# Optimization experiments

Hardware: AMD Instinct MI355X
Metric: run time of the kernel (lower is better)

The kernel has to match this reference:

```python
import jax, jax.numpy as jnp
import numpy as np

N = 10000      # nodes (= num_spatial_nodes)
E = 320000     # edges
IN = 4         # in_channels
HID = 256      # hidden_channels
H1, C1 = 4, 64 # conv1: heads, per-head out (hidden//heads)
EDIM = 1       # edge_feature_size
EPS = 1e-5


def _layernorm(x, g, b):
    mu = jnp.mean(x, axis=-1, keepdims=True)
    var = jnp.mean(jnp.square(x - mu), axis=-1, keepdims=True)
    return (x - mu) / jnp.sqrt(var + EPS) * g + b


def _gatv2(x, src, dst, ea, Wl, bl, Wr, br, We, att, bias, H, C, n):
    # PyG GATv2Conv: lin_l on source, lin_r on target, lin_edge on edge_attr
    xl = (x @ Wl + bl).reshape(n, H, C)
    xr = (x @ Wr + br).reshape(n, H, C)
    ee = (ea @ We).reshape(-1, H, C)
    m = jax.nn.leaky_relu(xl[src] + xr[dst] + ee, 0.2)   # [E', H, C]
    logit = jnp.einsum('ehc,hc->eh', m, att)             # [E', H]
    # segment softmax over incoming edges of each dst node
    mx = jax.ops.segment_max(logit, dst, num_segments=n)
    ex = jnp.exp(logit - mx[dst])
    den = jax.ops.segment_sum(ex, dst, num_segments=n)
    alpha = ex / den[dst]
    out = jax.ops.segment_sum(xl[src] * alpha[:, :, None], dst, num_segments=n)
    return out.reshape(n, H * C) + bias


def setup_inputs() -> dict:
    key = jax.random.key(0)
    ks = jax.random.split(key, 32)
    gl = lambda k, shape, fan: (jax.random.normal(k, shape, jnp.float32) / np.sqrt(fan)).astype(jnp.float32)
    inp = {}
    inp['x'] = jax.random.normal(ks[0], (N, IN), jnp.float32)
    inp['edge_index'] = jax.random.randint(ks[1], (2, E), 0, N, jnp.int32)
    inp['edge_attr'] = jax.random.normal(ks[2], (E, EDIM), jnp.float32)
    # conv1 (heads=4, out=64, concat -> 256)
    inp['Wl1'] = gl(ks[3], (IN, HID), IN);  inp['bl1'] = jnp.zeros((HID,), jnp.float32)
    inp['Wr1'] = gl(ks[4], (IN, HID), IN);  inp['br1'] = jnp.zeros((HID,), jnp.float32)
    inp['We1'] = gl(ks[5], (EDIM, HID), EDIM)
    inp['att1'] = gl(ks[6], (H1, C1), C1)
    inp['bias1'] = jnp.zeros((HID,), jnp.float32)
    inp['g1'] = jnp.ones((HID,), jnp.float32); inp['be1'] = jnp.zeros((HID,), jnp.float32)
    # conv2 (heads=1, out=256)
    inp['Wl2'] = gl(ks[7], (HID, HID), HID); inp['bl2'] = jnp.zeros((HID,), jnp.float32)
    inp['Wr2'] = gl(ks[8], (HID, HID), HID); inp['br2'] = jnp.zeros((HID,), jnp.float32)
    inp['We2'] = gl(ks[9], (EDIM, HID), EDIM)
    inp['att2'] = gl(ks[10], (1, HID), HID)
    inp['bias2'] = jnp.zeros((HID,), jnp.float32)
    inp['g2'] = jnp.ones((HID,), jnp.float32); inp['be2'] = jnp.zeros((HID,), jnp.float32)
    # policy head
    inp['Wp1'] = gl(ks[11], (HID, HID // 2), HID); inp['bp1'] = jnp.zeros((HID // 2,), jnp.float32)
    inp['Wp2'] = gl(ks[12], (HID // 2, IN), HID // 2); inp['bp2'] = jnp.zeros((IN,), jnp.float32)
    return inp


def reference(x, edge_index, edge_attr,
              Wl1, bl1, Wr1, br1, We1, att1, bias1, g1, be1,
              Wl2, bl2, Wr2, br2, We2, att2, bias2, g2, be2,
              Wp1, bp1, Wp2, bp2):
    src, dst = edge_index[0], edge_index[1]
    # add_self_loops with fill_value='mean': loop edge_attr = mean of incoming edge_attr
    deg = jax.ops.segment_sum(jnp.ones((E,), jnp.float32), dst, num_segments=N)
    loop_attr = jax.ops.segment_sum(edge_attr, dst, num_segments=N) / jnp.maximum(deg, 1.0)[:, None]
    ar = jnp.arange(N, dtype=src.dtype)
    src_a = jnp.concatenate([src, ar]); dst_a = jnp.concatenate([dst, ar])
    ea_a = jnp.concatenate([edge_attr, loop_attr], axis=0)
    h = _gatv2(x, src_a, dst_a, ea_a, Wl1, bl1, Wr1, br1, We1, att1, bias1, H1, C1, N)
    h = jax.nn.relu(_layernorm(h, g1, be1))
    h = _gatv2(h, src_a, dst_a, ea_a, Wl2, bl2, Wr2, br2, We2, att2, bias2, 1, HID, N)
    h = jax.nn.relu(_layernorm(h, g2, be2))
    logits = jax.nn.relu(h @ Wp1 + bp1) @ Wp2 + bp2   # [N, IN]
    return jax.nn.softmax(logits.reshape(1, -1), axis=1)
```

## Files before the change

### kernel.cpp

```cpp
#include <hip/hip_runtime.h>
#include <math.h>

#define N_NODES 10000
#define N_EDGES 320000
#define N_AUG   (N_EDGES + N_NODES)
#define CPK_CAP 330752
#define HID     256

typedef short short8 __attribute__((ext_vector_type(8)));
typedef float floatx16 __attribute__((ext_vector_type(16)));

static __device__ __forceinline__ unsigned bf16rne(float f) {
  unsigned u = __float_as_uint(f);
  return (u + 0x7FFFu + ((u >> 16) & 1u)) >> 16;
}

__global__ void k_deg(const int* __restrict__ dst, const float* __restrict__ ea,
                      int* __restrict__ deg, float* __restrict__ asum) {
  int e = blockIdx.x * blockDim.x + threadIdx.x;
  if (e < N_EDGES) {
    int d = dst[e];
    atomicAdd(&deg[d], 1);
    atomicAdd(&asum[d], ea[e]);
  }
}

__global__ void __launch_bounds__(256) k_scan(
    const int* __restrict__ deg, const float* __restrict__ asum,
    int* __restrict__ offs, float* __restrict__ lattr) {
  __shared__ int wsum[4];
  int t = threadIdx.x;
  int base = t * 40;
  int s = 0;
  for (int i = 0; i < 40; i++) {
    int n = base + i;
    if (n < N_NODES) s += deg[n] + 1;
  }
  int v = s;
  #pragma unroll
  for (int d = 1; d < 64; d <<= 1) {
    int u = __shfl_up(v, d);
    if ((t & 63) >= d) v += u;
  }
  if ((t & 63) == 63) wsum[t >> 6] = v;
  __syncthreads();
  int wb = 0;
  for (int i = 0; i < (t >> 6); i++) wb += wsum[i];
  int run = wb + v - s;
  for (int i = 0; i < 40; i++) {
    int n = base + i;
    if (n < N_NODES) {
      offs[n] = run;
      int d = deg[n];
      run += d + 1;
      lattr[n] = asum[n] / (float)max(d, 1);
    }
  }
  if (t == 255) offs[N_NODES] = wb + v;
}

__global__ void k_scatter(const int* __restrict__ src, const int* __restrict__ dst,
                          const float* __restrict__ ea, const float* __restrict__ lattr,
                          const int* __restrict__ offs, int* __restrict__ cursor,
                          int2* __restrict__ cpk) {
  int e = blockIdx.x * blockDim.x + threadIdx.x;
  if (e >= N_AUG) {
    if (e < CPK_CAP) cpk[e] = make_int2(0, 0);
    return;
  }
  int s, d; float a;
  if (e < N_EDGES) { s = src[e]; d = dst[e]; a = ea[e]; }
  else             { s = e - N_EDGES; d = s; a = lattr[s]; }
  int pos = offs[d] + atomicAdd(&cursor[d], 1);
  cpk[pos] = make_int2(s, __float_as_int(a));
}

__global__ void __launch_bounds__(256) k_cvtw(
    const float* __restrict__ W1, const float* __restrict__ W2,
    unsigned short* __restrict__ Wt) {
  __shared__ float tile[32][33];
  const float* W = blockIdx.z ? W2 : W1;
  int rowoff = blockIdx.z * 256;
  int kb = blockIdx.x * 32, nb = blockIdx.y * 32;
  int t = threadIdx.x;
  int tx = t & 31, ty = t >> 5;
  #pragma unroll
  for (int rep = 0; rep < 4; rep++)
    tile[ty + 8*rep][tx] = W[(kb + ty + 8*rep)*HID + nb + tx];
  __syncthreads();
  #pragma unroll
  for (int rep = 0; rep < 4; rep++) {
    int n = nb + ty + 8*rep;
    Wt[(rowoff + n)*256 + kb + tx] = (unsigned short)bf16rne(tile[tx][ty + 8*rep]);
  }
}

__global__ void __launch_bounds__(256) k_cvtwp(
    const float* __restrict__ Wp1, unsigned short* __restrict__ Wp1t) {
  __shared__ float tile[32][33];
  int kb = blockIdx.x * 32, nb = blockIdx.y * 32;
  int t = threadIdx.x;
  int tx = t & 31, ty = t >> 5;
  #pragma unroll
  for (int rep = 0; rep < 4; rep++)
    tile[ty + 8*rep][tx] = Wp1[(kb + ty + 8*rep)*128 + nb + tx];
  __syncthreads();
  #pragma unroll
  for (int rep = 0; rep < 4; rep++) {
    int n = nb + ty + 8*rep;
    Wp1t[n*256 + kb + tx] = (unsigned short)bf16rne(tile[tx][ty + 8*rep]);
  }
}

#define C1_EDGE(xs, av, l0, l1, l2, l3, p)                                              \
  {                                                                                     \
    l0 = fmaf(xs.x,wl0.x, fmaf(xs.y,wl1.x, fmaf(xs.z,wl2.x, fmaf(xs.w,wl3.x, blv.x)))); \
    l1 = fmaf(xs.x,wl0.y, fmaf(xs.y,wl1.y, fmaf(xs.z,wl2.y, fmaf(xs.w,wl3.y, blv.y)))); \
    l2 = fmaf(xs.x,wl0.z, fmaf(xs.y,wl1.z, fmaf(xs.z,wl2.z, fmaf(xs.w,wl3.z, blv.z)))); \
    l3 = fmaf(xs.x,wl0.w, fmaf(xs.y,wl1.w, fmaf(xs.z,wl2.w, fmaf(xs.w,wl3.w, blv.w)))); \
    float m0 = l0 + fmaf(av, we.x, r4.x); m0 = fmaxf(m0, 0.2f*m0);                      \
    float m1 = l1 + fmaf(av, we.y, r4.y); m1 = fmaxf(m1, 0.2f*m1);                      \
    float m2 = l2 + fmaf(av, we.z, r4.z); m2 = fmaxf(m2, 0.2f*m2);                      \
    float m3 = l3 + fmaf(av, we.w, r4.w); m3 = fmaxf(m3, 0.2f*m3);                      \
    p = m0*at.x + m1*at.y + m2*at.z + m3*at.w;                                          \
  }

#define C1_PROC8()                                                              \
  {                                                                             \
    float4 xA = *(const float4*)&x[eA.x*4];                                     \
    float4 xB = *(const float4*)&x[eB.x*4];                                     \
    float4 xC = *(const float4*)&x[eC.x*4];                                     \
    float4 xD = *(const float4*)&x[eD.x*4];                                     \
    float4 xE = *(const float4*)&x[eE.x*4];                                     \
    float4 xF = *(const float4*)&x[eF.x*4];                                     \
    float4 xG = *(const float4*)&x[eG.x*4];                                     \
    float4 xH = *(const float4*)&x[eH.x*4];                                     \
    float avA = __int_as_float(eA.y), avB = __int_as_float(eB.y);               \
    float avC = __int_as_float(eC.y), avD = __int_as_float(eD.y);               \
    float avE = __int_as_float(eE.y), avF = __int_as_float(eF.y);               \
    float avG = __int_as_float(eG.y), avH = __int_as_float(eH.y);               \
    float lA0,lA1,lA2,lA3,pA, lB0,lB1,lB2,lB3,pB;                               \
    float lC0,lC1,lC2,lC3,pC, lD0,lD1,lD2,lD3,pD;                               \
    float lE0,lE1,lE2,lE3,pE, lF0,lF1,lF2,lF3,pF;                               \
    float lG0,lG1,lG2,lG3,pG, lH0,lH1,lH2,lH3,pH;                               \
    C1_EDGE(xA, avA, lA0,lA1,lA2,lA3, pA);                                      \
    C1_EDGE(xB, avB, lB0,lB1,lB2,lB3, pB);                                      \
    C1_EDGE(xC, avC, lC0,lC1,lC2,lC3, pC);                                      \
    C1_EDGE(xD, avD, lD0,lD1,lD2,lD3, pD);                                      \
    C1_EDGE(xE, avE, lE0,lE1,lE2,lE3, pE);                                      \
    C1_EDGE(xF, avF, lF0,lF1,lF2,lF3, pF);                                      \
    C1_EDGE(xG, avG, lG0,lG1,lG2,lG3, pG);                                      \
    C1_EDGE(xH, avH, lH0,lH1,lH2,lH3, pH);                                      \
    float sAB = b1 ? pA : pB, kAB = b1 ? pB : pA;                               \
    float qAB = kAB + __shfl_xor(sAB, 1);                                       \
    float sCD = b1 ? pC : pD, kCD = b1 ? pD : pC;                               \
    float qCD = kCD + __shfl_xor(sCD, 1);                                       \
    float sEF = b1 ? pE : pF, kEF = b1 ? pF : pE;                               \
    float qEF = kEF + __shfl_xor(sEF, 1);                                       \
    float sGH = b1 ? pG : pH, kGH = b1 ? pH : pG;                               \
    float qGH = kGH + __shfl_xor(sGH, 1);                                       \
    float u0s = b2 ? qAB : qCD, u0k = b2 ? qCD : qAB;                           \
    float u0 = u0k + __shfl_xor(u0s, 2);                                        \
    float u1s = b2 ? qEF : qGH, u1k = b2 ? qGH : qEF;                           \
    float u1 = u1k + __shfl_xor(u1s, 2);                                        \
    float vvs = b4 ? u0 : u1, vvk = b4 ? u1 : u0;                               \
    float vv = vvk + __shfl_xor(vvs, 4);                                        \
    vv += __shfl_xor(vv, 8);                                                    \
    float exv = expf(vv);                                                       \
    float xAe = __shfl(exv, 0, 16), xBe = __shfl(exv, 1, 16);                   \
    float xCe = __shfl(exv, 2, 16), xDe = __shfl(exv, 3, 16);                   \
    float xEe = __shfl(exv, 4, 16), xFe = __shfl(exv, 5, 16);                   \
    float xGe = __shfl(exv, 6, 16), xHe = __shfl(exv, 7, 16);                   \
    D += ((xAe + xBe) + (xCe + xDe)) + ((xEe + xFe) + (xGe + xHe));             \
    a0 = fmaf(xDe, lD0, fmaf(xCe, lC0, fmaf(xBe, lB0, fmaf(xAe, lA0, a0))));    \
    a0 = fmaf(xHe, lH0, fmaf(xGe, lG0, fmaf(xFe, lF0, fmaf(xEe, lE0, a0))));    \
    a1 = fmaf(xDe, lD1, fmaf(xCe, lC1, fmaf(xBe, lB1, fmaf(xAe, lA1, a1))));    \
    a1 = fmaf(xHe, lH1, fmaf(xGe, lG1, fmaf(xFe, lF1, fmaf(xEe, lE1, a1))));    \
    a2 = fmaf(xDe, lD2, fmaf(xCe, lC2, fmaf(xBe, lB2, fmaf(xAe, lA2, a2))));    \
    a2 = fmaf(xHe, lH2, fmaf(xGe, lG2, fmaf(xFe, lF2, fmaf(xEe, lE2, a2))));    \
    a3 = fmaf(xDe, lD3, fmaf(xCe, lC3, fmaf(xBe, lB3, fmaf(xAe, lA3, a3))));    \
    a3 = fmaf(xHe, lH3, fmaf(xGe, lG3, fmaf(xFe, lF3, fmaf(xEe, lE3, a3))));    \
  }

__global__ void __launch_bounds__(256) k_conv1(
    const float* __restrict__ x,
    const float* __restrict__ Wl, const float* __restrict__ bl,
    const float* __restrict__ Wr, const float* __restrict__ br,
    const float* __restrict__ We, const float* __restrict__ att,
    const int* __restrict__ offs, const int2* __restrict__ cpk,
    const float* __restrict__ bias, const float* __restrict__ g,
    const float* __restrict__ be, uint2* __restrict__ h1b) {
  int t = threadIdx.x;
  int n = blockIdx.x * 4 + (t >> 6);
  int c = 4 * (t & 63);
  bool b1 = (t & 1) != 0, b2 = (t & 2) != 0, b4 = (t & 4) != 0;

  float4 wl0 = *(const float4*)&Wl[0*HID + c];
  float4 wl1 = *(const float4*)&Wl[1*HID + c];
  float4 wl2 = *(const float4*)&Wl[2*HID + c];
  float4 wl3 = *(const float4*)&Wl[3*HID + c];
  float4 blv = *(const float4*)&bl[c];
  float4 we  = *(const float4*)&We[c];
  float4 at  = *(const float4*)&att[c];

  float4 xn = *(const float4*)&x[n*4];
  float4 r4;
  {
    float4 wr0 = *(const float4*)&Wr[0*HID + c];
    float4 wr1 = *(const float4*)&Wr[1*HID + c];
    float4 wr2 = *(const float4*)&Wr[2*HID + c];
    float4 wr3 = *(const float4*)&Wr[3*HID + c];
    float4 brv = *(const float4*)&br[c];
    r4.x = fmaf(xn.x,wr0.x, fmaf(xn.y,wr1.x, fmaf(xn.z,wr2.x, fmaf(xn.w,wr3.x, brv.x))));
    r4.y = fmaf(xn.x,wr0.y, fmaf(xn.y,wr1.y, fmaf(xn.z,wr2.y, fmaf(xn.w,wr3.y, brv.y))));
    r4.z = fmaf(xn.x,wr0.z, fmaf(xn.y,wr1.z, fmaf(xn.z,wr2.z, fmaf(xn.w,wr3.z, brv.z))));
    r4.w = fmaf(xn.x,wr0.w, fmaf(xn.y,wr1.w, fmaf(xn.z,wr2.w, fmaf(xn.w,wr3.w, brv.w))));
  }

  int js = __builtin_amdgcn_readfirstlane(offs[n]);
  int je = __builtin_amdgcn_readfirstlane(offs[n+1]);

  float D = 0.f, a0 = 0.f, a1 = 0.f, a2 = 0.f, a3 = 0.f;

  int j = js;
  if (j + 7 < je) {
    int2 eA = cpk[j],   eB = cpk[j+1], eC = cpk[j+2], eD = cpk[j+3];
    int2 eE = cpk[j+4], eF = cpk[j+5], eG = cpk[j+6], eH = cpk[j+7];
    for (; j + 7 < je; j += 8) {
      int2 nA = cpk[j+8],  nB = cpk[j+9],  nC = cpk[j+10], nD = cpk[j+11];
      int2 nE = cpk[j+12], nF = cpk[j+13], nG = cpk[j+14], nH = cpk[j+15];
      C1_PROC8();
      eA = nA; eB = nB; eC = nC; eD = nD;
      eE = nE; eF = nF; eG = nG; eH = nH;
    }
  }
  for (; j < je; j++) {
    int2 eA = cpk[j];
    float4 xA = *(const float4*)&x[eA.x*4];
    float avA = __int_as_float(eA.y);
    float lA0,lA1,lA2,lA3,pA;
    C1_EDGE(xA, avA, lA0,lA1,lA2,lA3, pA);
    #pragma unroll
    for (int msk = 1; msk < 16; msk <<= 1) pA += __shfl_xor(pA, msk);
    float eAx = expf(pA);
    D += eAx;
    a0 = fmaf(eAx, lA0, a0);
    a1 = fmaf(eAx, lA1, a1);
    a2 = fmaf(eAx, lA2, a2);
    a3 = fmaf(eAx, lA3, a3);
  }

  float inv = 1.f / D;
  float4 b4v = *(const float4*)&bias[c];
  float o0 = fmaf(a0, inv, b4v.x);
  float o1 = fmaf(a1, inv, b4v.y);
  float o2 = fmaf(a2, inv, b4v.z);
  float o3 = fmaf(a3, inv, b4v.w);

  float s = o0 + o1 + o2 + o3;
  #pragma unroll
  for (int msk = 1; msk < 64; msk <<= 1) s += __shfl_xor(s, msk);
  float mu = s * (1.f / 256.f);
  float d0 = o0 - mu, d1 = o1 - mu, d2 = o2 - mu, d3 = o3 - mu;
  float sq = d0*d0 + d1*d1 + d2*d2 + d3*d3;
  #pragma unroll
  for (int msk = 1; msk < 64; msk <<= 1) sq += __shfl_xor(sq, msk);
  float rstd = rsqrtf(sq * (1.f / 256.f) + 1e-5f);
  float4 g4  = *(const float4*)&g[c];
  float4 be4 = *(const float4*)&be[c];
  float oy0 = fmaxf(fmaf(d0 * rstd, g4.x, be4.x), 0.f);
  float oy1 = fmaxf(fmaf(d1 * rstd, g4.y, be4.y), 0.f);
  float oy2 = fmaxf(fmaf(d2 * rstd, g4.z, be4.z), 0.f);
  float oy3 = fmaxf(fmaf(d3 * rstd, g4.w, be4.w), 0.f);
  uint2 pk;
  pk.x = bf16rne(oy0) | (bf16rne(oy1) << 16);
  pk.y = bf16rne(oy2) | (bf16rne(oy3) << 16);
  h1b[n*64 + (t & 63)] = pk;
}

#define C2_LOAD(q, xs)                                  \
  float4 xs;                                            \
  xs.x = __uint_as_float(q.x << 16);                    \
  xs.y = __uint_as_float(q.x & 0xFFFF0000u);            \
  xs.z = __uint_as_float(q.y << 16);                    \
  xs.w = __uint_as_float(q.y & 0xFFFF0000u);

#define C2_EDGE(xs, av, p)                                           \
  {                                                                  \
    float m0 = xs.x + fmaf(av, we.x, r4.x); m0 = fmaxf(m0, 0.2f*m0); \
    float m1 = xs.y + fmaf(av, we.y, r4.y); m1 = fmaxf(m1, 0.2f*m1); \
    float m2 = xs.z + fmaf(av, we.z, r4.z); m2 = fmaxf(m2, 0.2f*m2); \
    float m3 = xs.w + fmaf(av, we.w, r4.w); m3 = fmaxf(m3, 0.2f*m3); \
    p = m0*at.x + m1*at.y + m2*at.z + m3*at.w;                       \
  }

#define C2_PROC8()                                                              \
  {                                                                             \
    C2_LOAD(q0, xs0); C2_LOAD(q1, xs1); C2_LOAD(q2, xs2); C2_LOAD(q3, xs3);     \
    C2_LOAD(q4, xs4); C2_LOAD(q5, xs5); C2_LOAD(q6, xs6); C2_LOAD(q7, xs7);     \
    float av0 = __int_as_float(e0.y), av1 = __int_as_float(e1.y);               \
    float av2 = __int_as_float(e2.y), av3 = __int_as_float(e3.y);               \
    float av4 = __int_as_float(e4.y), av5 = __int_as_float(e5.y);               \
    float av6 = __int_as_float(e6.y), av7 = __int_as_float(e7.y);               \
    float p0,p1,p2,p3,p4,p5,p6,p7;                                              \
    C2_EDGE(xs0, av0, p0); C2_EDGE(xs1, av1, p1);                               \
    C2_EDGE(xs2, av2, p2); C2_EDGE(xs3, av3, p3);                               \
    C2_EDGE(xs4, av4, p4); C2_EDGE(xs5, av5, p5);                               \
    C2_EDGE(xs6, av6, p6); C2_EDGE(xs7, av7, p7);                               \
    float sAB = b1 ? p0 : p1, kAB = b1 ? p1 : p0;                               \
    float qAB = kAB + __shfl_xor(sAB, 1);                                       \
    float sCD = b1 ? p2 : p3, kCD = b1 ? p3 : p2;                               \
    float qCD = kCD + __shfl_xor(sCD, 1);                                       \
    float sEF = b1 ? p4 : p5, kEF = b1 ? p5 : p4;                               \
    float qEF = kEF + __shfl_xor(sEF, 1);                                       \
    float sGH = b1 ? p6 : p7, kGH = b1 ? p7 : p6;                               \
    float qGH = kGH + __shfl_xor(sGH, 1);                                       \
    float u0s = b2 ? qAB : qCD, u0k = b2 ? qCD : qAB;                           \
    float u0 = u0k + __shfl_xor(u0s, 2);                                        \
    float u1s = b2 ? qEF : qGH, u1k = b2 ? qGH : qEF;                           \
    float u1 = u1k + __shfl_xor(u1s, 2);                                        \
    float vvs = b4 ? u0 : u1, vvk = b4 ? u1 : u0;                               \
    float vv = vvk + __shfl_xor(vvs, 4);                                        \
    vv += __shfl_xor(vv, 8);                                                    \
    vv += __shfl_xor(vv, 16);                                                   \
    vv += __shfl_xor(vv, 32);                                                   \
    float exv = expf(vv);                                                       \
    float x0 = __shfl(exv, 0), x1 = __shfl(exv, 1);                             \
    float x2 = __shfl(exv, 2), x3 = __shfl(exv, 3);                             \
    float x4 = __shfl(exv, 4), x5 = __shfl(exv, 5);                             \
    float x6 = __shfl(exv, 6), x7 = __shfl(exv, 7);                             \
    D += ((x0 + x1) + (x2 + x3)) + ((x4 + x5) + (x6 + x7));                     \
    a0 = fmaf(x3, xs3.x, fmaf(x2, xs2.x, fmaf(x1, xs1.x, fmaf(x0, xs0.x, a0))));\
    a0 = fmaf(x7, xs7.x, fmaf(x6, xs6.x, fmaf(x5, xs5.x, fmaf(x4, xs4.x, a0))));\
    a1 = fmaf(x3, xs3.y, fmaf(x2, xs2.y, fmaf(x1, xs1.y, fmaf(x0, xs0.y, a1))));\
    a1 = fmaf(x7, xs7.y, fmaf(x6, xs6.y, fmaf(x5, xs5.y, fmaf(x4, xs4.y, a1))));\
    a2 = fmaf(x3, xs3.z, fmaf(x2, xs2.z, fmaf(x1, xs1.z, fmaf(x0, xs0.z, a2))));\
    a2 = fmaf(x7, xs7.z, fmaf(x6, xs6.z, fmaf(x5, xs5.z, fmaf(x4, xs4.z, a2))));\
    a3 = fmaf(x3, xs3.w, fmaf(x2, xs2.w, fmaf(x1, xs1.w, fmaf(x0, xs0.w, a3))));\
    a3 = fmaf(x7, xs7.w, fmaf(x6, xs6.w, fmaf(x5, xs5.w, fmaf(x4, xs4.w, a3))));\
  }

__global__ void __launch_bounds__(256) k_conv2(
    const uint2* __restrict__ xlb, const float* __restrict__ xr,
    const int* __restrict__ offs, const int2* __restrict__ cpk,
    const float* __restrict__ We, const float* __restrict__ att,
    const float* __restrict__ bias, const float* __restrict__ g,
    const float* __restrict__ be, uint2* __restrict__ h2b) {
  int t = threadIdx.x;
  int n = blockIdx.x * 4 + (t >> 6);
  int lane = t & 63;
  int c = 4 * lane;
  bool b1 = (t & 1) != 0, b2 = (t & 2) != 0, b4 = (t & 4) != 0;
  float4 r4 = *(const float4*)&xr[n*HID + c];
  float4 we = *(const float4*)&We[c];
  float4 at = *(const float4*)&att[c];
  int js = __builtin_amdgcn_readfirstlane(offs[n]);
  int je = __builtin_amdgcn_readfirstlane(offs[n+1]);

  float D = 0.f, a0 = 0.f, a1 = 0.f, a2 = 0.f, a3 = 0.f;

  int j = js;
  if (je - js >= 16) {
    int2 e0 = cpk[j],   e1 = cpk[j+1], e2 = cpk[j+2], e3 = cpk[j+3];
    int2 e4 = cpk[j+4], e5 = cpk[j+5], e6 = cpk[j+6], e7 = cpk[j+7];
    int2 f0 = cpk[j+8],  f1 = cpk[j+9],  f2 = cpk[j+10], f3 = cpk[j+11];
    int2 f4 = cpk[j+12], f5 = cpk[j+13], f6 = cpk[j+14], f7 = cpk[j+15];
    uint2 q0 = xlb[e0.x*64 + lane];
    uint2 q1 = xlb[e1.x*64 + lane];
    uint2 q2 = xlb[e2.x*64 + lane];
    uint2 q3 = xlb[e3.x*64 + lane];
    uint2 q4 = xlb[e4.x*64 + lane];
    uint2 q5 = xlb[e5.x*64 + lane];
    uint2 q6 = xlb[e6.x*64 + lane];
    uint2 q7 = xlb[e7.x*64 + lane];
    for (; j + 15 < je; j += 8) {
      uint2 r0 = xlb[f0.x*64 + lane];
      uint2 r1 = xlb[f1.x*64 + lane];
      uint2 r2 = xlb[f2.x*64 + lane];
      uint2 r3 = xlb[f3.x*64 + lane];
      uint2 r4_ = xlb[f4.x*64 + lane];
      uint2 r5 = xlb[f5.x*64 + lane];
      uint2 r6 = xlb[f6.x*64 + lane];
      uint2 r7 = xlb[f7.x*64 + lane];
      int2 g0 = cpk[j+16], g1 = cpk[j+17], g2 = cpk[j+18], g3 = cpk[j+19];
      int2 g4 = cpk[j+20], g5 = cpk[j+21], g6 = cpk[j+22], g7 = cpk[j+23];
      C2_PROC8();
      e0 = f0; e1 = f1; e2 = f2; e3 = f3; e4 = f4; e5 = f5; e6 = f6; e7 = f7;
      f0 = g0; f1 = g1; f2 = g2; f3 = g3; f4 = g4; f5 = g5; f6 = g6; f7 = g7;
      q0 = r0; q1 = r1; q2 = r2; q3 = r3; q4 = r4_; q5 = r5; q6 = r6; q7 = r7;
    }
    C2_PROC8();
    j += 8;
  }
  for (; j + 7 < je; j += 8) {
    int2 e0 = cpk[j],   e1 = cpk[j+1], e2 = cpk[j+2], e3 = cpk[j+3];
    int2 e4 = cpk[j+4], e5 = cpk[j+5], e6 = cpk[j+6], e7 = cpk[j+7];
    uint2 q0 = xlb[e0.x*64 + lane];
    uint2 q1 = xlb[e1.x*64 + lane];
    uint2 q2 = xlb[e2.x*64 + lane];
    uint2 q3 = xlb[e3.x*64 + lane];
    uint2 q4 = xlb[e4.x*64 + lane];
    uint2 q5 = xlb[e5.x*64 + lane];
    uint2 q6 = xlb[e6.x*64 + lane];
    uint2 q7 = xlb[e7.x*64 + lane];
    C2_PROC8();
  }
  for (; j < je; j++) {
    int2 e0 = cpk[j];
    float av0 = __int_as_float(e0.y);
    uint2 q0 = xlb[e0.x*64 + lane];
    C2_LOAD(q0, xs0);
    float p0;
    C2_EDGE(xs0, av0, p0);
    #pragma unroll
    for (int msk = 1; msk < 64; msk <<= 1) p0 += __shfl_xor(p0, msk);
    float x0 = expf(p0);
    D += x0;
    a0 = fmaf(x0, xs0.x, a0);
    a1 = fmaf(x0, xs0.y, a1);
    a2 = fmaf(x0, xs0.z, a2);
    a3 = fmaf(x0, xs0.w, a3);
  }

  float inv = 1.f / D;
  float4 b4v = *(const float4*)&bias[c];
  float o0 = fmaf(a0, inv, b4v.x);
  float o1 = fmaf(a1, inv, b4v.y);
  float o2 = fmaf(a2, inv, b4v.z);
  float o3 = fmaf(a3, inv, b4v.w);

  float s = o0 + o1 + o2 + o3;
  #pragma unroll
  for (int msk = 1; msk < 64; msk <<= 1) s += __shfl_xor(s, msk);
  float mu = s * (1.f / 256.f);
  float d0 = o0 - mu, d1 = o1 - mu, d2 = o2 - mu, d3 = o3 - mu;
  float sq = d0*d0 + d1*d1 + d2*d2 + d3*d3;
  #pragma unroll
  for (int msk = 1; msk < 64; msk <<= 1) sq += __shfl_xor(sq, msk);
  float rstd = rsqrtf(sq * (1.f / 256.f) + 1e-5f);
  float4 g4  = *(const float4*)&g[c];
  float4 be4 = *(const float4*)&be[c];
  float oy0 = fmaxf(fmaf(d0 * rstd, g4.x, be4.x), 0.f);
  float oy1 = fmaxf(fmaf(d1 * rstd, g4.y, be4.y), 0.f);
  float oy2 = fmaxf(fmaf(d2 * rstd, g4.z, be4.z), 0.f);
  float oy3 = fmaxf(fmaf(d3 * rstd, g4.w, be4.w), 0.f);
  uint2 pk;
  pk.x = bf16rne(oy0) | (bf16rne(oy1) << 16);
  pk.y = bf16rne(oy2) | (bf16rne(oy3) << 16);
  h2b[n*64 + lane] = pk;
}

__global__ void __launch_bounds__(256) k_gemm_dual(
    const unsigned short* __restrict__ h1b, const unsigned short* __restrict__ Wt,
    const float* __restrict__ b1, const float* __restrict__ b2,
    unsigned short* __restrict__ O1b, float* __restrict__ O2) {
  __shared__ unsigned short A_lds[64][72];
  __shared__ unsigned short W_lds[128][72];
  int t = threadIdx.x;
  int r0 = blockIdx.x * 64;
  int nb0 = blockIdx.y * 128;
  int l = t & 63;
  int wave = t >> 6;
  int wr = wave >> 1, wc = wave & 1;

  floatx16 acc[2] = {{0}, {0}};

  int sar = t >> 2, sak = (t & 3) * 16;
  int arow = min(r0 + sar, N_NODES - 1);
  int swn = t >> 1, swk = (t & 1) * 32;
  const unsigned short* Wrow = &Wt[(nb0 + swn) * 256];

  for (int kb = 0; kb < 256; kb += 64) {
    uint4 av0 = *(const uint4*)&h1b[arow*256 + kb + sak];
    uint4 av1 = *(const uint4*)&h1b[arow*256 + kb + sak + 8];
    uint4 wv0 = *(const uint4*)&Wrow[kb + swk];
    uint4 wv1 = *(const uint4*)&Wrow[kb + swk + 8];
    uint4 wv2 = *(const uint4*)&Wrow[kb + swk + 16];
    uint4 wv3 = *(const uint4*)&Wrow[kb + swk + 24];
    __syncthreads();
    *(uint4*)&A_lds[sar][sak]     = av0;
    *(uint4*)&A_lds[sar][sak + 8] = av1;
    *(uint4*)&W_lds[swn][swk]      = wv0;
    *(uint4*)&W_lds[swn][swk +  8] = wv1;
    *(uint4*)&W_lds[swn][swk + 16] = wv2;
    *(uint4*)&W_lds[swn][swk + 24] = wv3;
    __syncthreads();
    #pragma unroll
    for (int ks = 0; ks < 64; ks += 16) {
      short8 af  = *(const short8*)&A_lds[wr*32 + (l & 31)][ks + 8*(l >> 5)];
      short8 bf0 = *(const short8*)&W_lds[wc*64      + (l & 31)][ks + 8*(l >> 5)];
      short8 bf1 = *(const short8*)&W_lds[wc*64 + 32 + (l & 31)][ks + 8*(l >> 5)];
      acc[0] = __builtin_amdgcn_mfma_f32_32x32x16_bf16(af, bf0, acc[0], 0, 0, 0);
      acc[1] = __builtin_amdgcn_mfma_f32_32x32x16_bf16(af, bf1, acc[1], 0, 0, 0);
    }
  }

  bool isO1 = (nb0 < 256);
  #pragma unroll
  for (int tile = 0; tile < 2; tile++) {
    int col = nb0 + wc*64 + tile*32 + (l & 31);
    float bias = isO1 ? b1[col] : b2[col - 256];
    #pragma unroll
    for (int reg = 0; reg < 16; reg++) {
      int row = (reg & 3) + 8*(reg >> 2) + 4*(l >> 5);
      int r = r0 + wr*32 + row;
      if (r < N_NODES) {
        float v = acc[tile][reg] + bias;
        if (isO1) O1b[r*256 + col] = (unsigned short)bf16rne(v);
        else      O2[r*256 + (col - 256)] = v;
      }
    }
  }
}

__global__ void __launch_bounds__(256) k_policy(
    const unsigned short* __restrict__ h2b, const unsigned short* __restrict__ Wp1t,
    const float* __restrict__ bp1, const float* __restrict__ Wp2,
    const float* __restrict__ bp2, float* __restrict__ elg, float* __restrict__ tot) {
  __shared__ __align__(16) char smembuf[64 * 132 * 4];
  unsigned short* A_lds = (unsigned short*)smembuf;
  unsigned short* W_lds = (unsigned short*)(smembuf + 64*72*2);
  float* hidl = (float*)smembuf;
  __shared__ float wred[4];
  int t = threadIdx.x;
  int r0 = blockIdx.x * 64;
  int l = t & 63;
  int wave = t >> 6;
  int wr = wave >> 1, wc = wave & 1;

  floatx16 acc[2] = {{0}, {0}};

  int sar = t >> 2, sak = (t & 3) * 16;
  int arow = min(r0 + sar, N_NODES - 1);
  int swn = t >> 1, swk = (t & 1) * 32;
  const unsigned short* Wrow = &Wp1t[swn * 256];

  for (int kb = 0; kb < 256; kb += 64) {
    uint4 av0 = *(const uint4*)&h2b[arow*256 + kb + sak];
    uint4 av1 = *(const uint4*)&h2b[arow*256 + kb + sak + 8];
    uint4 wv0 = *(const uint4*)&Wrow[kb + swk];
    uint4 wv1 = *(const uint4*)&Wrow[kb + swk + 8];
    uint4 wv2 = *(const uint4*)&Wrow[kb + swk + 16];
    uint4 wv3 = *(const uint4*)&Wrow[kb + swk + 24];
    __syncthreads();
    *(uint4*)&A_lds[sar*72 + sak]     = av0;
    *(uint4*)&A_lds[sar*72 + sak + 8] = av1;
    *(uint4*)&W_lds[swn*72 + swk]      = wv0;
    *(uint4*)&W_lds[swn*72 + swk +  8] = wv1;
    *(uint4*)&W_lds[swn*72 + swk + 16] = wv2;
    *(uint4*)&W_lds[swn*72 + swk + 24] = wv3;
    __syncthreads();
    #pragma unroll
    for (int ks = 0; ks < 64; ks += 16) {
      short8 af  = *(const short8*)&A_lds[(wr*32 + (l & 31))*72 + ks + 8*(l >> 5)];
      short8 bf0 = *(const short8*)&W_lds[(wc*64      + (l & 31))*72 + ks + 8*(l >> 5)];
      short8 bf1 = *(const short8*)&W_lds[(wc*64 + 32 + (l & 31))*72 + ks + 8*(l >> 5)];
      acc[0] = __builtin_amdgcn_mfma_f32_32x32x16_bf16(af, bf0, acc[0], 0, 0, 0);
      acc[1] = __builtin_amdgcn_mfma_f32_32x32x16_bf16(af, bf1, acc[1], 0, 0, 0);
    }
  }
  __syncthreads();
  #pragma unroll
  for (int tile = 0; tile < 2; tile++) {
    int col = wc*64 + tile*32 + (l & 31);
    float bias = bp1[col];
    #pragma unroll
    for (int reg = 0; reg < 16; reg++) {
      int row = (reg & 3) + 8*(reg >> 2) + 4*(l >> 5) + wr*32;
      hidl[row*132 + col] = fmaxf(acc[tile][reg] + bias, 0.f);
    }
  }
  __syncthreads();
  int nl = t >> 2, i = t & 3;
  float s = bp2[i];
  for (int k = 0; k < 128; k += 4) {
    float4 hv = *(const float4*)&hidl[nl*132 + k];
    s = fmaf(hv.x, Wp2[(k+0)*4 + i],
        fmaf(hv.y, Wp2[(k+1)*4 + i],
        fmaf(hv.z, Wp2[(k+2)*4 + i],
        fmaf(hv.w, Wp2[(k+3)*4 + i], s))));
  }
  int n = r0 + nl;
  float esum = 0.f;
  if (n < N_NODES) {
    float e = expf(s);
    elg[n*4 + i] = e;
    esum = e;
  }
  #pragma unroll
  for (int msk = 1; msk < 64; msk <<= 1) esum += __shfl_xor(esum, msk);
  if ((t & 63) == 0) wred[t >> 6] = esum;
  __syncthreads();
  if (t == 0) atomicAdd(tot, (wred[0] + wred[1]) + (wred[2] + wred[3]));
}

__global__ void __launch_bounds__(1024) k_sm_final(const float* __restrict__ elg,
                                                   const float* __restrict__ tot,
                                                   float* __restrict__ out) {
  int i = blockIdx.x * 1024 + threadIdx.x;
  float inv = 1.f / tot[0];
  if (i < N_NODES * 4) out[i] = elg[i] * inv;
}

extern "C" void kernel_launch(void* const* d_in, const int* in_sizes, int n_in,
                              void* d_out, int out_size, void* d_ws, size_t ws_size,
                              hipStream_t stream) {
  const float* x    = (const float*)d_in[0];
  const int*   ei   = (const int*)  d_in[1];
  const float* ea   = (const float*)d_in[2];
  const float* Wl1  = (const float*)d_in[3];
  const float* bl1  = (const float*)d_in[4];
  const float* Wr1  = (const float*)d_in[5];
  const float* br1  = (const float*)d_in[6];
  const float* We1  = (const float*)d_in[7];
  const float* att1 = (const float*)d_in[8];
  const float* bias1= (const float*)d_in[9];
  const float* g1   = (const float*)d_in[10];
  const float* be1  = (const float*)d_in[11];
  const float* Wl2  = (const float*)d_in[12];
  const float* bl2  = (const float*)d_in[13];
  const float* Wr2  = (const float*)d_in[14];
  const float* br2  = (const float*)d_in[15];
  const float* We2  = (const float*)d_in[16];
  const float* att2 = (const float*)d_in[17];
  const float* bias2= (const float*)d_in[18];
  const float* g2   = (const float*)d_in[19];
  const float* be2  = (const float*)d_in[20];
  const float* Wp1  = (const float*)d_in[21];
  const float* bp1  = (const float*)d_in[22];
  const float* Wp2  = (const float*)d_in[23];
  const float* bp2  = (const float*)d_in[24];
  float* out = (float*)d_out;

  const int* srcp = ei;
  const int* dstp = ei + N_EDGES;

  int*   deg    = (int*)d_ws;
  int*   cursor = deg + 10240;
  float* asum   = (float*)(cursor + 10240);
  float* tot    = asum + 10240;
  int*   offs   = (int*)(tot + 16);
  float* lattr  = (float*)(offs + 10240);
  int2*  cpk    = (int2*)(lattr + 10240);
  unsigned short* h1b = (unsigned short*)(cpk + CPK_CAP);
  unsigned short* h2b = h1b;
  unsigned short* xl2bf = h1b + 2560000;
  float* xr2    = (float*)(xl2bf + 2560000);
  float* elg    = xr2 + 2560000;
  unsigned short* Wt   = (unsigned short*)(elg + 40960);
  unsigned short* Wp1t = Wt + 512*256;

  hipMemsetAsync(deg, 0, (3 * 10240 + 16) * sizeof(int), stream);

  k_cvtw   <<<dim3(8, 8, 2), 256, 0, stream>>>(Wl2, Wr2, Wt);
  k_cvtwp  <<<dim3(8, 4), 256, 0, stream>>>(Wp1, Wp1t);
  k_deg    <<<(N_EDGES + 255)/256, 256, 0, stream>>>(dstp, ea, deg, asum);
  k_scan   <<<1, 256, 0, stream>>>(deg, asum, offs, lattr);
  k_scatter<<<(CPK_CAP + 255)/256, 256, 0, stream>>>(srcp, dstp, ea, lattr, offs,
                                                     cursor, cpk);
  k_conv1  <<<N_NODES/4, 256, 0, stream>>>(x, Wl1, bl1, Wr1, br1, We1, att1,
                                           offs, cpk, bias1, g1, be1, (uint2*)h1b);
  k_gemm_dual<<<dim3(157, 4), 256, 0, stream>>>(h1b, Wt, bl2, br2, xl2bf, xr2);
  k_conv2  <<<N_NODES/4, 256, 0, stream>>>((const uint2*)xl2bf, xr2, offs, cpk,
                                           We2, att2, bias2, g2, be2, (uint2*)h2b);
  k_policy <<<157, 256, 0, stream>>>(h2b, Wp1t, bp1, Wp2, bp2, elg, tot);
  k_sm_final<<<40, 1024, 0, stream>>>(elg, tot, out);
}
```

Baseline: 306.2 us.

## Reuse degree-atomic ranks for CSR scatter, merge weight prep, software-pipeline conv1 gathers

New measurement: 287.9 us. 1.06x faster.

```diff
diff --git a/kernel.cpp b/kernel.cpp
--- a/kernel.cpp
+++ b/kernel.cpp
@@ -16,11 +16,12 @@
 }
 
 __global__ void k_deg(const int* __restrict__ dst, const float* __restrict__ ea,
-                      int* __restrict__ deg, float* __restrict__ asum) {
+                      int* __restrict__ deg, float* __restrict__ asum,
+                      int* __restrict__ rank) {
   int e = blockIdx.x * blockDim.x + threadIdx.x;
   if (e < N_EDGES) {
     int d = dst[e];
-    atomicAdd(&deg[d], 1);
+    rank[e] = atomicAdd(&deg[d], 1);
     atomicAdd(&asum[d], ea[e]);
   }
 }
@@ -61,54 +62,59 @@
 
 __global__ void k_scatter(const int* __restrict__ src, const int* __restrict__ dst,
                           const float* __restrict__ ea, const float* __restrict__ lattr,
-                          const int* __restrict__ offs, int* __restrict__ cursor,
+                          const int* __restrict__ offs, const int* __restrict__ rank,
                           int2* __restrict__ cpk) {
   int e = blockIdx.x * blockDim.x + threadIdx.x;
   if (e >= N_AUG) {
     if (e < CPK_CAP) cpk[e] = make_int2(0, 0);
     return;
   }
-  int s, d; float a;
-  if (e < N_EDGES) { s = src[e]; d = dst[e]; a = ea[e]; }
-  else             { s = e - N_EDGES; d = s; a = lattr[s]; }
-  int pos = offs[d] + atomicAdd(&cursor[d], 1);
+  int pos, s; float a;
+  if (e < N_EDGES) {
+    s = src[e];
+    int d = dst[e];
+    a = ea[e];
+    pos = offs[d] + rank[e];
+  } else {
+    s = e - N_EDGES;
+    a = lattr[s];
+    pos = offs[s + 1] - 1;
+  }
   cpk[pos] = make_int2(s, __float_as_int(a));
 }
 
-__global__ void __launch_bounds__(256) k_cvtw(
+__global__ void __launch_bounds__(256) k_prep(
     const float* __restrict__ W1, const float* __restrict__ W2,
-    unsigned short* __restrict__ Wt) {
+    const float* __restrict__ Wp1,
+    unsigned short* __restrict__ Wt, unsigned short* __restrict__ Wp1t) {
   __shared__ float tile[32][33];
-  const float* W = blockIdx.z ? W2 : W1;
-  int rowoff = blockIdx.z * 256;
+  int z = blockIdx.z;
   int kb = blockIdx.x * 32, nb = blockIdx.y * 32;
   int t = threadIdx.x;
   int tx = t & 31, ty = t >> 5;
-  #pragma unroll
-  for (int rep = 0; rep < 4; rep++)
-    tile[ty + 8*rep][tx] = W[(kb + ty + 8*rep)*HID + nb + tx];
-  __syncthreads();
-  #pragma unroll
-  for (int rep = 0; rep < 4; rep++) {
-    int n = nb + ty + 8*rep;
-    Wt[(rowoff + n)*256 + kb + tx] = (unsigned short)bf16rne(tile[tx][ty + 8*rep]);
-  }
-}
-
-__global__ void __launch_bounds__(256) k_cvtwp(
-    const float* __restrict__ Wp1, unsigned short* __restrict__ Wp1t) {
-  __shared__ float tile[32][33];
-  int kb = blockIdx.x * 32, nb = blockIdx.y * 32;
-  int t = threadIdx.x;
-  int tx = t & 31, ty = t >> 5;
-  #pragma unroll
-  for (int rep = 0; rep < 4; rep++)
-    tile[ty + 8*rep][tx] = Wp1[(kb + ty + 8*rep)*128 + nb + tx];
-  __syncthreads();
-  #pragma unroll
-  for (int rep = 0; rep < 4; rep++) {
-    int n = nb + ty + 8*rep;
-    Wp1t[n*256 + kb + tx] = (unsigned short)bf16rne(tile[tx][ty + 8*rep]);
+  if (z < 2) {
+    const float* W = z ? W2 : W1;
+    int rowoff = z * 256;
+    #pragma unroll
+    for (int rep = 0; rep < 4; rep++)
+      tile[ty + 8*rep][tx] = W[(kb + ty + 8*rep)*HID + nb + tx];
+    __syncthreads();
+    #pragma unroll
+    for (int rep = 0; rep < 4; rep++) {
+      int n = nb + ty + 8*rep;
+      Wt[(rowoff + n)*256 + kb + tx] = (unsigned short)bf16rne(tile[tx][ty + 8*rep]);
+    }
+  } else {
+    if (nb >= 128) return;
+    #pragma unroll
+    for (int rep = 0; rep < 4; rep++)
+      tile[ty + 8*rep][tx] = Wp1[(kb + ty + 8*rep)*128 + nb + tx];
+    __syncthreads();
+    #pragma unroll
+    for (int rep = 0; rep < 4; rep++) {
+      int n = nb + ty + 8*rep;
+      Wp1t[n*256 + kb + tx] = (unsigned short)bf16rne(tile[tx][ty + 8*rep]);
+    }
   }
 }
 
@@ -125,16 +131,8 @@
     p = m0*at.x + m1*at.y + m2*at.z + m3*at.w;                                          \
   }
 
-#define C1_PROC8()                                                              \
+#define C1_BODY8()                                                              \
   {                                                                             \
-    float4 xA = *(const float4*)&x[eA.x*4];                                     \
-    float4 xB = *(const float4*)&x[eB.x*4];                                     \
-    float4 xC = *(const float4*)&x[eC.x*4];                                     \
-    float4 xD = *(const float4*)&x[eD.x*4];                                     \
-    float4 xE = *(const float4*)&x[eE.x*4];                                     \
-    float4 xF = *(const float4*)&x[eF.x*4];                                     \
-    float4 xG = *(const float4*)&x[eG.x*4];                                     \
-    float4 xH = *(const float4*)&x[eH.x*4];                                     \
     float avA = __int_as_float(eA.y), avB = __int_as_float(eB.y);               \
     float avC = __int_as_float(eC.y), avD = __int_as_float(eD.y);               \
     float avE = __int_as_float(eE.y), avF = __int_as_float(eF.y);               \
@@ -223,16 +221,50 @@
   float D = 0.f, a0 = 0.f, a1 = 0.f, a2 = 0.f, a3 = 0.f;
 
   int j = js;
-  if (j + 7 < je) {
+  if (je - js >= 16) {
     int2 eA = cpk[j],   eB = cpk[j+1], eC = cpk[j+2], eD = cpk[j+3];
     int2 eE = cpk[j+4], eF = cpk[j+5], eG = cpk[j+6], eH = cpk[j+7];
-    for (; j + 7 < je; j += 8) {
-      int2 nA = cpk[j+8],  nB = cpk[j+9],  nC = cpk[j+10], nD = cpk[j+11];
-      int2 nE = cpk[j+12], nF = cpk[j+13], nG = cpk[j+14], nH = cpk[j+15];
-      C1_PROC8();
-      eA = nA; eB = nB; eC = nC; eD = nD;
-      eE = nE; eF = nF; eG = nG; eH = nH;
-    }
+    int2 fA = cpk[j+8],  fB = cpk[j+9],  fC = cpk[j+10], fD = cpk[j+11];
+    int2 fE = cpk[j+12], fF = cpk[j+13], fG = cpk[j+14], fH = cpk[j+15];
+    float4 xA = *(const float4*)&x[eA.x*4];
+    float4 xB = *(const float4*)&x[eB.x*4];
+    float4 xC = *(const float4*)&x[eC.x*4];
+    float4 xD = *(const float4*)&x[eD.x*4];
+    float4 xE = *(const float4*)&x[eE.x*4];
+    float4 xF = *(const float4*)&x[eF.x*4];
+    float4 xG = *(const float4*)&x[eG.x*4];
+    float4 xH = *(const float4*)&x[eH.x*4];
+    for (; j + 15 < je; j += 8) {
+      float4 yA = *(const float4*)&x[fA.x*4];
+      float4 yB = *(const float4*)&x[fB.x*4];
+      float4 yC = *(const float4*)&x[fC.x*4];
+      float4 yD = *(const float4*)&x[fD.x*4];
+      float4 yE = *(const float4*)&x[fE.x*4];
+      float4 yF = *(const float4*)&x[fF.x*4];
+      float4 yG = *(const float4*)&x[fG.x*4];
+      float4 yH = *(const float4*)&x[fH.x*4];
+      int2 gA = cpk[j+16], gB = cpk[j+17], gC = cpk[j+18], gD = cpk[j+19];
+      int2 gE = cpk[j+20], gF = cpk[j+21], gG = cpk[j+22], gH = cpk[j+23];
+      C1_BODY8();
+      eA = fA; eB = fB; eC = fC; eD = fD; eE = fE; eF = fF; eG = fG; eH = fH;
+      fA = gA; fB = gB; fC = gC; fD = gD; fE = gE; fF = gF; fG = gG; fH = gH;
+      xA = yA; xB = yB; xC = yC; xD = yD; xE = yE; xF = yF; xG = yG; xH = yH;
+    }
+    C1_BODY8();
+    j += 8;
+  }
+  for (; j + 7 < je; j += 8) {
+    int2 eA = cpk[j],   eB = cpk[j+1], eC = cpk[j+2], eD = cpk[j+3];
+    int2 eE = cpk[j+4], eF = cpk[j+5], eG = cpk[j+6], eH = cpk[j+7];
+    float4 xA = *(const float4*)&x[eA.x*4];
+    float4 xB = *(const float4*)&x[eB.x*4];
+    float4 xC = *(const float4*)&x[eC.x*4];
+    float4 xD = *(const float4*)&x[eD.x*4];
+    float4 xE = *(const float4*)&x[eE.x*4];
+    float4 xF = *(const float4*)&x[eF.x*4];
+    float4 xG = *(const float4*)&x[eG.x*4];
+    float4 xH = *(const float4*)&x[eH.x*4];
+    C1_BODY8();
   }
   for (; j < je; j++) {
     int2 eA = cpk[j];
@@ -636,12 +668,12 @@
   const int* dstp = ei + N_EDGES;
 
   int*   deg    = (int*)d_ws;
-  int*   cursor = deg + 10240;
-  float* asum   = (float*)(cursor + 10240);
+  float* asum   = (float*)(deg + 10240);
   float* tot    = asum + 10240;
   int*   offs   = (int*)(tot + 16);
   float* lattr  = (float*)(offs + 10240);
-  int2*  cpk    = (int2*)(lattr + 10240);
+  int*   rank   = (int*)(lattr + 10240);
+  int2*  cpk    = (int2*)(rank + 320192);
   unsigned short* h1b = (unsigned short*)(cpk + CPK_CAP);
   unsigned short* h2b = h1b;
   unsigned short* xl2bf = h1b + 2560000;
@@ -650,14 +682,13 @@
   unsigned short* Wt   = (unsigned short*)(elg + 40960);
   unsigned short* Wp1t = Wt + 512*256;
 
-  hipMemsetAsync(deg, 0, (3 * 10240 + 16) * sizeof(int), stream);
-
-  k_cvtw   <<<dim3(8, 8, 2), 256, 0, stream>>>(Wl2, Wr2, Wt);
-  k_cvtwp  <<<dim3(8, 4), 256, 0, stream>>>(Wp1, Wp1t);
-  k_deg    <<<(N_EDGES + 255)/256, 256, 0, stream>>>(dstp, ea, deg, asum);
+  hipMemsetAsync(deg, 0, (2 * 10240 + 16) * sizeof(int), stream);
+
+  k_prep   <<<dim3(8, 8, 3), 256, 0, stream>>>(Wl2, Wr2, Wp1, Wt, Wp1t);
+  k_deg    <<<(N_EDGES + 255)/256, 256, 0, stream>>>(dstp, ea, deg, asum, rank);
   k_scan   <<<1, 256, 0, stream>>>(deg, asum, offs, lattr);
   k_scatter<<<(CPK_CAP + 255)/256, 256, 0, stream>>>(srcp, dstp, ea, lattr, offs,
-                                                     cursor, cpk);
+                                                     rank, cpk);
   k_conv1  <<<N_NODES/4, 256, 0, stream>>>(x, Wl1, bl1, Wr1, br1, We1, att1,
                                            offs, cpk, bias1, g1, be1, (uint2*)h1b);
   k_gemm_dual<<<dim3(157, 4), 256, 0, stream>>>(h1b, Wt, bl2, br2, xl2bf, xr2);
```
